# Performance work log

Measured on AMD Instinct MI355X. Metric: run time of the kernel, lower is better.

Reference implementation:

```python
import jax, jax.numpy as jnp
import numpy as np


def setup_inputs() -> dict:
    key = jax.random.key(0)
    k1, k2, k3 = jax.random.split(key, 3)
    B, L, H = 4, 4096, 1024
    x = jax.random.normal(k1, (B, L, H), dtype=jnp.float32)
    # 0.02 scale keeps attention logits in a sane range (like trained weights)
    in_proj_weight = jax.random.normal(k2, (3 * H, H), dtype=jnp.float32) * 0.02
    in_proj_bias = jnp.zeros((3 * H,), dtype=jnp.float32)
    out_proj_weight = jax.random.normal(k3, (H, H), dtype=jnp.float32) * 0.02
    out_proj_bias = jnp.zeros((H,), dtype=jnp.float32)
    return {
        "x": x,
        "in_proj_weight": in_proj_weight,
        "in_proj_bias": in_proj_bias,
        "out_proj_weight": out_proj_weight,
        "out_proj_bias": out_proj_bias,
        "num_heads": 16,
        "window_size": 128,
    }


def _windowed_mha(x, in_proj_weight, in_proj_bias, out_proj_weight, out_proj_bias,
                  num_heads, window_size):
    B, L, H = x.shape
    P = window_size
    pad = (-L) % P  # static
    xp = jnp.pad(x, ((0, 0), (0, pad), (0, 0))) if pad else x
    Lp = xp.shape[1]
    nw = Lp // P
    w = xp.reshape(B * nw, P, H)  # [NW, P, H]
    # packed QKV projection (torch MHA: q,k,v = split(x @ W_in.T + b_in))
    qkv = jnp.einsum('nph,dh->npd', w, in_proj_weight) + in_proj_bias
    q, k, v = jnp.split(qkv, 3, axis=-1)
    hd = H // num_heads

    def to_heads(t):
        return t.reshape(B * nw, P, num_heads, hd).transpose(0, 2, 1, 3)  # [NW, Hh, P, hd]

    q, k, v = to_heads(q), to_heads(k), to_heads(v)
    scale = 1.0 / jnp.sqrt(jnp.asarray(hd, dtype=x.dtype))
    scores = jnp.einsum('nhqd,nhkd->nhqk', q * scale, k)  # [NW, Hh, P, P]
    attn = jax.nn.softmax(scores, axis=-1)
    o = jnp.einsum('nhqk,nhkd->nhqd', attn, v)  # [NW, Hh, P, hd]
    o = o.transpose(0, 2, 1, 3).reshape(B * nw, P, H)
    o = jnp.einsum('nph,oh->npo', o, out_proj_weight) + out_proj_bias
    o = o.reshape(B, Lp, H)
    return o[:, :L]


def reference(x, in_proj_weight, in_proj_bias, out_proj_weight, out_proj_bias,
              num_heads, window_size):
    return _windowed_mha(x, in_proj_weight, in_proj_bias, out_proj_weight,
                         out_proj_bias, num_heads, window_size)
```

## Files before the change

### kernel.cpp

```cpp
#include <hip/hip_runtime.h>
#include <hip/hip_bf16.h>
#include <cstdint>


typedef __bf16 bf16_t;
typedef __bf16 bf16x8 __attribute__((ext_vector_type(8)));
typedef __bf16 bf16x4 __attribute__((ext_vector_type(4)));
typedef float  floatx4 __attribute__((ext_vector_type(4)));

#define MFMA_16x16x32(A, B, C) __builtin_amdgcn_mfma_f32_16x16x32_bf16(A, B, C, 0, 0, 0)

__device__ __forceinline__ void gld_lds16(const bf16_t* g, bf16_t* l) {
  __builtin_amdgcn_global_load_lds(
      (__attribute__((address_space(1))) void*)(void*)(g),
      (__attribute__((address_space(3))) void*)(l), 16, 0, 0);
}

__global__ void cvt_f32_to_bf16(const float* __restrict__ src,
                                bf16_t* __restrict__ dst, int n8) {
  int i = blockIdx.x * blockDim.x + threadIdx.x;
  if (i >= n8) return;
  const float4* s4 = (const float4*)src;
  float4 a = s4[2 * (size_t)i];
  float4 b = s4[2 * (size_t)i + 1];
  bf16x8 o;
  o[0] = (bf16_t)a.x; o[1] = (bf16_t)a.y; o[2] = (bf16_t)a.z; o[3] = (bf16_t)a.w;
  o[4] = (bf16_t)b.x; o[5] = (bf16_t)b.y; o[6] = (bf16_t)b.z; o[7] = (bf16_t)b.w;
  *(bf16x8*)(dst + (size_t)i * 8) = o;
}

__global__ void cvt_repack_win(const float* __restrict__ Win,
                               bf16_t* __restrict__ Wpk) {
  const int dr = blockIdx.x;
  const int head = dr / 192, s = dr - head * 192;
  const int src = (s < 64) ? head * 64 + s
                : (s < 128) ? 1024 + head * 64 + (s - 64)
                            : 2048 + head * 64 + (s - 128);
  const float4* srow = (const float4*)(Win + (size_t)src * 1024);
  const int i = threadIdx.x;
  float4 a = srow[2 * i];
  float4 b = srow[2 * i + 1];
  bf16x8 o;
  o[0] = (bf16_t)a.x; o[1] = (bf16_t)a.y; o[2] = (bf16_t)a.z; o[3] = (bf16_t)a.w;
  o[4] = (bf16_t)b.x; o[5] = (bf16_t)b.y; o[6] = (bf16_t)b.z; o[7] = (bf16_t)b.w;
  *(bf16x8*)(Wpk + (size_t)dr * 1024 + i * 8) = o;
}

template <bool F32OUT>
__global__ __launch_bounds__(256, 2) void gemm_bt(
    const bf16_t* __restrict__ A, const bf16_t* __restrict__ Bm,
    const float* __restrict__ bias, void* __restrict__ Cp,
    int M, int N, int K) {
  __shared__ bf16_t As[128 * 32];
  __shared__ bf16_t Bs[128 * 32];
  const int tid  = threadIdx.x;
  const int lane = tid & 63;
  const int wave = tid >> 6;
  const int n16  = lane & 15;
  const int q4   = lane >> 4;
  const int wm   = (wave >> 1) * 64;
  const int wn   = (wave & 1) * 64;
  const int m0   = blockIdx.y * 128;
  const int n0   = blockIdx.x * 128;

  floatx4 acc[4][4] = {};

  for (int k0 = 0; k0 < K; k0 += 32) {
    __syncthreads();
#pragma unroll
    for (int it = 0; it < 2; ++it) {
      const int ch = it * 256 + wave * 64 + lane;
      const int r = ch >> 2, c = (ch & 3) * 8;
      gld_lds16(A + (size_t)(m0 + r) * K + k0 + c,
                As + (size_t)(it * 256 + wave * 64) * 8);
      gld_lds16(Bm + (size_t)(n0 + r) * K + k0 + c,
                Bs + (size_t)(it * 256 + wave * 64) * 8);
    }
    __syncthreads();

    bf16x8 af[4], bfr[4];
#pragma unroll
    for (int i = 0; i < 4; ++i)
      af[i] = *(const bf16x8*)&As[(wm + i * 16 + n16) * 32 + q4 * 8];
#pragma unroll
    for (int j = 0; j < 4; ++j)
      bfr[j] = *(const bf16x8*)&Bs[(wn + j * 16 + n16) * 32 + q4 * 8];
#pragma unroll
    for (int i = 0; i < 4; ++i)
#pragma unroll
      for (int j = 0; j < 4; ++j)
        acc[i][j] = MFMA_16x16x32(af[i], bfr[j], acc[i][j]);
  }

#pragma unroll
  for (int i = 0; i < 4; ++i)
#pragma unroll
    for (int j = 0; j < 4; ++j) {
      const int col = n0 + wn + j * 16 + n16;
      const float b = bias[col];
#pragma unroll
      for (int r = 0; r < 4; ++r) {
        const int row = m0 + wm + i * 16 + q4 * 4 + r;
        const float v = acc[i][j][r] + b;
        if (F32OUT)
          ((float*)Cp)[(size_t)row * N + col] = v;
        else
          ((bf16_t*)Cp)[(size_t)row * N + col] = (bf16_t)v;
      }
    }
}

__global__ __launch_bounds__(256, 3) void qkv_attn(
    const bf16_t* __restrict__ X,
    const bf16_t* __restrict__ Wpk,
    const float* __restrict__ bin,
    bf16_t* __restrict__ o)
{
  __shared__ bf16_t smem[26624];
  bf16_t* Xs  = smem;
  bf16_t* Ws  = smem + 4096;
  bf16_t* qs  = smem;
  bf16_t* ks  = smem + 9216;
  bf16_t* vsT = smem + 18432;
  bf16_t* Ps  = smem;

  const int wid  = blockIdx.x;
  const int h    = blockIdx.y;
  const int tid  = threadIdx.x;
  const int lane = tid & 63;
  const int wave = tid >> 6;
  const int n16  = lane & 15;
  const int q4   = lane >> 4;
  const int wm   = (wave >> 1) * 64;
  const int wn   = (wave & 1) * 96;

  const bf16_t* Xg = X + (size_t)wid * 128 * 1024;
  const bf16_t* Wg = Wpk + (size_t)h * 192 * 1024;

  floatx4 acc[4][6] = {};
  for (int k0 = 0; k0 < 1024; k0 += 32) {
    __syncthreads();
#pragma unroll
    for (int it = 0; it < 2; ++it) {
      const int ch = it * 256 + wave * 64 + lane;
      gld_lds16(Xg + (size_t)(ch >> 2) * 1024 + k0 + (ch & 3) * 8,
                Xs + (it * 256 + wave * 64) * 8);
    }
#pragma unroll
    for (int it = 0; it < 3; ++it) {
      const int ch = it * 256 + wave * 64 + lane;
      gld_lds16(Wg + (size_t)(ch >> 2) * 1024 + k0 + (ch & 3) * 8,
                Ws + (it * 256 + wave * 64) * 8);
    }
    __syncthreads();

    bf16x8 af[4], bfr[6];
#pragma unroll
    for (int i = 0; i < 4; ++i)
      af[i] = *(const bf16x8*)&Xs[(wm + i * 16 + n16) * 32 + q4 * 8];
#pragma unroll
    for (int j = 0; j < 6; ++j)
      bfr[j] = *(const bf16x8*)&Ws[(wn + j * 16 + n16) * 32 + q4 * 8];
#pragma unroll
    for (int i = 0; i < 4; ++i)
#pragma unroll
      for (int j = 0; j < 6; ++j)
        acc[i][j] = MFMA_16x16x32(af[i], bfr[j], acc[i][j]);
  }
  __syncthreads();

#pragma unroll
  for (int j = 0; j < 6; ++j) {
    const int base = wn + j * 16;
    const int col  = base + n16;
    const int gb = (base < 64) ? h * 64 + col
                 : (base < 128) ? 1024 + h * 64 + (col - 64)
                                : 2048 + h * 64 + (col - 128);
    const float bias = bin[gb];
#pragma unroll
    for (int i = 0; i < 4; ++i) {
      const int row0 = wm + i * 16 + q4 * 4;
      if (base < 64) {
#pragma unroll
        for (int r = 0; r < 4; ++r)
          qs[(row0 + r) * 72 + col] = (bf16_t)((acc[i][j][r] + bias) * 0.125f);
      } else if (base < 128) {
#pragma unroll
        for (int r = 0; r < 4; ++r)
          ks[(row0 + r) * 72 + (col - 64)] = (bf16_t)(acc[i][j][r] + bias);
      } else {
        bf16x4 pv;
#pragma unroll
        for (int r = 0; r < 4; ++r) pv[r] = (bf16_t)(acc[i][j][r] + bias);
        const int d = col - 128;
        const int c8 = row0 >> 3, pos = row0 & 7;
        *(bf16x4*)&vsT[d * 128 + ((c8 ^ n16) << 3) + pos] = pv;
      }
    }
  }
  __syncthreads();

  floatx4 sacc[2][8] = {};
#pragma unroll
  for (int ks0 = 0; ks0 < 2; ++ks0) {
    bf16x8 aq[2];
#pragma unroll
    for (int i = 0; i < 2; ++i)
      aq[i] = *(const bf16x8*)&qs[(wave * 32 + i * 16 + n16) * 72 + ks0 * 32 + q4 * 8];
#pragma unroll
    for (int j = 0; j < 8; ++j) {
      bf16x8 bk = *(const bf16x8*)&ks[(j * 16 + n16) * 72 + ks0 * 32 + q4 * 8];
      sacc[0][j] = MFMA_16x16x32(aq[0], bk, sacc[0][j]);
      sacc[1][j] = MFMA_16x16x32(aq[1], bk, sacc[1][j]);
    }
  }
  __syncthreads();

  float invs[2][4];
#pragma unroll
  for (int i = 0; i < 2; ++i) {
#pragma unroll
    for (int r = 0; r < 4; ++r) {
      float vals[8];
      float s = 0.f;
#pragma unroll
      for (int j = 0; j < 8; ++j) {
        vals[j] = __expf(sacc[i][j][r]);
        s += vals[j];
      }
      for (int m = 1; m < 16; m <<= 1) s += __shfl_xor(s, m, 64);
      invs[i][r] = 1.0f / s;
      const int prow = wave * 32 + i * 16 + q4 * 4 + r;
#pragma unroll
      for (int j = 0; j < 8; ++j)
        Ps[prow * 136 + j * 16 + n16] = (bf16_t)vals[j];
    }
  }
  __syncthreads();

  floatx4 oacc[2][4] = {};
#pragma unroll
  for (int kk = 0; kk < 4; ++kk) {
    bf16x8 ap[2];
#pragma unroll
    for (int i = 0; i < 2; ++i)
      ap[i] = *(const bf16x8*)&Ps[(wave * 32 + i * 16 + n16) * 136 + kk * 32 + q4 * 8];
#pragma unroll
    for (int j = 0; j < 4; ++j) {
      const int d = j * 16 + n16;
      bf16x8 bv = *(const bf16x8*)&vsT[d * 128 + (((kk * 4 + q4) ^ n16) << 3)];
      oacc[0][j] = MFMA_16x16x32(ap[0], bv, oacc[0][j]);
      oacc[1][j] = MFMA_16x16x32(ap[1], bv, oacc[1][j]);
    }
  }

  bf16_t* go = o + (size_t)wid * 128 * 1024 + h * 64;
#pragma unroll
  for (int i = 0; i < 2; ++i)
#pragma unroll
    for (int j = 0; j < 4; ++j)
#pragma unroll
      for (int r = 0; r < 4; ++r) {
        const int row = wave * 32 + i * 16 + q4 * 4 + r;
        go[(size_t)row * 1024 + j * 16 + n16] = (bf16_t)(oacc[i][j][r] * invs[i][r]);
      }
}

extern "C" void kernel_launch(void* const* d_in, const int* in_sizes, int n_in,
                              void* d_out, int out_size, void* d_ws, size_t ws_size,
                              hipStream_t stream) {
  const float* x    = (const float*)d_in[0];
  const float* Win  = (const float*)d_in[1];
  const float* bin  = (const float*)d_in[2];
  const float* Wout = (const float*)d_in[3];
  const float* bout = (const float*)d_in[4];
  float* out = (float*)d_out;

  const size_t M = 16384, H = 1024, H3 = 3072;

  bf16_t* xb    = (bf16_t*)d_ws;
  bf16_t* Wpk   = xb + M * H;
  bf16_t* Woutb = Wpk + H3 * H;
  bf16_t* ob    = Woutb + H * H;

  cvt_f32_to_bf16<<<dim3((unsigned)(M * H / 8 / 256)), 256, 0, stream>>>(
      x, xb, (int)(M * H / 8));
  cvt_repack_win<<<dim3((unsigned)H3), 128, 0, stream>>>(Win, Wpk);
  cvt_f32_to_bf16<<<dim3((unsigned)(H * H / 8 / 256)), 256, 0, stream>>>(
      Wout, Woutb, (int)(H * H / 8));

  qkv_attn<<<dim3(128, 16), 256, 0, stream>>>(xb, Wpk, bin, ob);

  gemm_bt<true><<<dim3((unsigned)(H / 128), (unsigned)(M / 128)), 256, 0, stream>>>(
      ob, Woutb, bout, out, (int)M, (int)H, (int)H);
}
```

Before: 308.6 us.

## Double K-tile depth to 64 with XOR-swizzled LDS layout in both GEMMs

```diff
diff --git a/kernel.cpp b/kernel.cpp
--- a/kernel.cpp
+++ b/kernel.cpp
@@ -47,12 +47,12 @@
 }
 
 template <bool F32OUT>
-__global__ __launch_bounds__(256, 2) void gemm_bt(
+__global__ __launch_bounds__(256, 3) void gemm_bt(
     const bf16_t* __restrict__ A, const bf16_t* __restrict__ Bm,
     const float* __restrict__ bias, void* __restrict__ Cp,
     int M, int N, int K) {
-  __shared__ bf16_t As[128 * 32];
-  __shared__ bf16_t Bs[128 * 32];
+  __shared__ bf16_t As[128 * 64];
+  __shared__ bf16_t Bs[128 * 64];
   const int tid  = threadIdx.x;
   const int lane = tid & 63;
   const int wave = tid >> 6;
@@ -65,31 +65,39 @@
 
   floatx4 acc[4][4] = {};
 
-  for (int k0 = 0; k0 < K; k0 += 32) {
+  for (int k0 = 0; k0 < K; k0 += 64) {
     __syncthreads();
 #pragma unroll
-    for (int it = 0; it < 2; ++it) {
-      const int ch = it * 256 + wave * 64 + lane;
-      const int r = ch >> 2, c = (ch & 3) * 8;
-      gld_lds16(A + (size_t)(m0 + r) * K + k0 + c,
-                As + (size_t)(it * 256 + wave * 64) * 8);
-      gld_lds16(Bm + (size_t)(n0 + r) * K + k0 + c,
-                Bs + (size_t)(it * 256 + wave * 64) * 8);
+    for (int it = 0; it < 4; ++it) {
+      const int ch = it * 256 + tid;
+      const int r  = ch >> 3;
+      const int c8 = (ch & 7) ^ (r & 7);
+      gld_lds16(A  + (size_t)(m0 + r) * K + k0 + c8 * 8,
+                As + (it * 256 + wave * 64) * 8);
+      gld_lds16(Bm + (size_t)(n0 + r) * K + k0 + c8 * 8,
+                Bs + (it * 256 + wave * 64) * 8);
     }
     __syncthreads();
 
-    bf16x8 af[4], bfr[4];
-#pragma unroll
-    for (int i = 0; i < 4; ++i)
-      af[i] = *(const bf16x8*)&As[(wm + i * 16 + n16) * 32 + q4 * 8];
-#pragma unroll
-    for (int j = 0; j < 4; ++j)
-      bfr[j] = *(const bf16x8*)&Bs[(wn + j * 16 + n16) * 32 + q4 * 8];
-#pragma unroll
-    for (int i = 0; i < 4; ++i)
-#pragma unroll
-      for (int j = 0; j < 4; ++j)
-        acc[i][j] = MFMA_16x16x32(af[i], bfr[j], acc[i][j]);
+#pragma unroll
+    for (int half = 0; half < 2; ++half) {
+      bf16x8 af[4], bfr[4];
+#pragma unroll
+      for (int i = 0; i < 4; ++i) {
+        const int row = wm + i * 16 + n16;
+        af[i] = *(const bf16x8*)&As[row * 64 + (((half * 4 + q4) ^ (row & 7)) * 8)];
+      }
+#pragma unroll
+      for (int j = 0; j < 4; ++j) {
+        const int row = wn + j * 16 + n16;
+        bfr[j] = *(const bf16x8*)&Bs[row * 64 + (((half * 4 + q4) ^ (row & 7)) * 8)];
+      }
+#pragma unroll
+      for (int i = 0; i < 4; ++i)
+#pragma unroll
+        for (int j = 0; j < 4; ++j)
+          acc[i][j] = MFMA_16x16x32(af[i], bfr[j], acc[i][j]);
+    }
   }
 
 #pragma unroll
@@ -118,7 +126,7 @@
 {
   __shared__ bf16_t smem[26624];
   bf16_t* Xs  = smem;
-  bf16_t* Ws  = smem + 4096;
+  bf16_t* Ws  = smem + 8192;
   bf16_t* qs  = smem;
   bf16_t* ks  = smem + 9216;
   bf16_t* vsT = smem + 18432;
@@ -138,34 +146,45 @@
   const bf16_t* Wg = Wpk + (size_t)h * 192 * 1024;
 
   floatx4 acc[4][6] = {};
-  for (int k0 = 0; k0 < 1024; k0 += 32) {
+  for (int k0 = 0; k0 < 1024; k0 += 64) {
     __syncthreads();
 #pragma unroll
-    for (int it = 0; it < 2; ++it) {
-      const int ch = it * 256 + wave * 64 + lane;
-      gld_lds16(Xg + (size_t)(ch >> 2) * 1024 + k0 + (ch & 3) * 8,
+    for (int it = 0; it < 4; ++it) {
+      const int ch = it * 256 + tid;
+      const int r  = ch >> 3;
+      const int c8 = (ch & 7) ^ (r & 7);
+      gld_lds16(Xg + (size_t)r * 1024 + k0 + c8 * 8,
                 Xs + (it * 256 + wave * 64) * 8);
     }
 #pragma unroll
-    for (int it = 0; it < 3; ++it) {
-      const int ch = it * 256 + wave * 64 + lane;
-      gld_lds16(Wg + (size_t)(ch >> 2) * 1024 + k0 + (ch & 3) * 8,
+    for (int it = 0; it < 6; ++it) {
+      const int ch = it * 256 + tid;
+      const int r  = ch >> 3;
+      const int c8 = (ch & 7) ^ (r & 7);
+      gld_lds16(Wg + (size_t)r * 1024 + k0 + c8 * 8,
                 Ws + (it * 256 + wave * 64) * 8);
     }
     __syncthreads();
 
-    bf16x8 af[4], bfr[6];
-#pragma unroll
-    for (int i = 0; i < 4; ++i)
-      af[i] = *(const bf16x8*)&Xs[(wm + i * 16 + n16) * 32 + q4 * 8];
-#pragma unroll
-    for (int j = 0; j < 6; ++j)
-      bfr[j] = *(const bf16x8*)&Ws[(wn + j * 16 + n16) * 32 + q4 * 8];
-#pragma unroll
-    for (int i = 0; i < 4; ++i)
-#pragma unroll
-      for (int j = 0; j < 6; ++j)
-        acc[i][j] = MFMA_16x16x32(af[i], bfr[j], acc[i][j]);
+#pragma unroll
+    for (int half = 0; half < 2; ++half) {
+      bf16x8 af[4], bfr[6];
+#pragma unroll
+      for (int i = 0; i < 4; ++i) {
+        const int row = wm + i * 16 + n16;
+        af[i] = *(const bf16x8*)&Xs[row * 64 + (((half * 4 + q4) ^ (row & 7)) * 8)];
+      }
+#pragma unroll
+      for (int j = 0; j < 6; ++j) {
+        const int row = wn + j * 16 + n16;
+        bfr[j] = *(const bf16x8*)&Ws[row * 64 + (((half * 4 + q4) ^ (row & 7)) * 8)];
+      }
+#pragma unroll
+      for (int i = 0; i < 4; ++i)
+#pragma unroll
+        for (int j = 0; j < 6; ++j)
+          acc[i][j] = MFMA_16x16x32(af[i], bfr[j], acc[i][j]);
+    }
   }
   __syncthreads();
 
```

Measured after the change: 291.3 us. 1.06x faster.
